# Optimization experiments

Hardware: AMD Instinct MI355X
Metric: run time of the kernel (lower is better)

## Reference

```python
import jax, jax.numpy as jnp
import numpy as np

NUM_CLASSES = 21
GAMMA = 2.0
LAMBDA_WGT = 1.0
EPS = 1e-6  # torch.nn.CosineSimilarity eps
B, C_FEAT, HF, WF = 16, 2048, 41, 41
H, W = 321, 321


def setup_inputs() -> dict:
    key = jax.random.key(0)
    k1, k2, k3, k4, k5 = jax.random.split(key, 5)
    return {
        "y_pred": jax.random.normal(k1, (B, NUM_CLASSES, H, W), dtype=jnp.float32),
        "ycrf": jax.random.randint(k2, (B, H, W), 0, NUM_CLASSES, dtype=jnp.int32),
        "yret": jax.random.randint(k3, (B, H, W), 0, NUM_CLASSES, dtype=jnp.int32),
        "feature_map": jax.random.normal(k4, (B, C_FEAT, HF, WF), dtype=jnp.float32),
        "classifier_weight": jax.random.normal(k5, (NUM_CLASSES, C_FEAT), dtype=jnp.float32),
    }


def reference(y_pred, ycrf, yret, feature_map, classifier_weight):
    K = NUM_CLASSES
    # softmax + log(softmax) fused as log_softmax (original does softmax then log)
    logp = jax.nn.log_softmax(y_pred, axis=1)                    # [B,K,H,W]
    # s_class[b,i,h,w] = (ycrf==i)&(yret==i): nonzero only at i==ycrf when ycrf==yret
    match = (ycrf == yret)                                       # [B,H,W]
    logp_c = jnp.take_along_axis(logp, ycrf[:, None], axis=1)[:, 0]  # [B,H,W] logp at class ycrf
    cnt = jnp.sum(match)
    loss_ce = -jnp.sum(jnp.where(match, logp_c, 0.0)) / cnt

    # correlation map: 1 + cosine(feature_map[b,:,h,w], classifier_weight[i]) at 41x41
    dots = jnp.einsum('bchw,kc->bkhw', feature_map, classifier_weight)   # [B,K,41,41]
    fn = jnp.sqrt(jnp.sum(feature_map * feature_map, axis=1, keepdims=True))  # [B,1,41,41]
    wn = jnp.sqrt(jnp.sum(classifier_weight * classifier_weight, axis=1))     # [K]
    denom_cos = jnp.maximum(fn * wn[None, :, None, None], EPS)
    corr = 1.0 + dots / denom_cos                                # [B,K,41,41]
    # bilinear upsample to 321x321, align_corners=False (half-pixel centers)
    corr_up = jax.image.resize(corr, (B, K, H, W), method='bilinear')
    # confidence map: (corr at class ycrf / max over classes)^gamma
    cstar = jnp.take_along_axis(corr_up, ycrf[:, None], axis=1)[:, 0]   # [B,H,W]
    conf = (cstar / jnp.max(corr_up, axis=1)) ** GAMMA                  # [B,H,W]

    # weighted CE over not_s_class: for each pixel, all classes except the matched one
    # sum_i not_s * conf * logp_i = conf*sum_i logp_i - match*conf*logp_{ycrf}
    m = match.astype(conf.dtype)
    sum_logp = jnp.sum(logp, axis=1)                             # [B,H,W]
    numer = jnp.sum(conf * sum_logp) - jnp.sum(m * conf * logp_c)
    denom = K * jnp.sum(conf) - jnp.sum(m * conf)
    loss_wce = -numer / denom
    return loss_ce + LAMBDA_WGT * loss_wce
```

## Files before the change

kernel.cpp:

```cpp
#include <hip/hip_runtime.h>
#include <math.h>

#define KCLS 21
#define BATCH 16
#define HF 41
#define WF 41
#define HH 321
#define WW 321
#define CFEAT 2048
#define HWF (HF*WF)
#define HWI (HH*WW)
#define NPIX (BATCH*HWI)
#define NBLK_C ((NPIX + 255)/256)
#define EPSC 1e-6f

__device__ float g_wn[KCLS];
__device__ float g_corr[(size_t)BATCH*KCLS*HWF];
__device__ float g_part[6][NBLK_C];

__global__ __launch_bounds__(256) void k_wn(const float* __restrict__ cw) {
    int wave = threadIdx.x >> 6, lane = threadIdx.x & 63;
    for (int k = wave; k < KCLS; k += 4) {
        float s = 0.f;
        for (int c = lane; c < CFEAT; c += 64) {
            float v = cw[k*CFEAT + c];
            s = fmaf(v, v, s);
        }
        #pragma unroll
        for (int off = 32; off; off >>= 1) s += __shfl_down(s, off, 64);
        if (lane == 0) g_wn[k] = sqrtf(s);
    }
}

__global__ __launch_bounds__(512) void k_corr(const float* __restrict__ fm,
                                              const float* __restrict__ cw) {
    int b = blockIdx.y;
    int lane = threadIdx.x & 63;
    int chunk = __builtin_amdgcn_readfirstlane(threadIdx.x >> 6);
    int hw = blockIdx.x * 64 + lane;
    bool valid = hw < HWF;
    const float* fbase = fm + (size_t)b * CFEAT * HWF + (valid ? hw : 0);
    int cbase = chunk * (CFEAT / 8);

    float acc[KCLS];
    #pragma unroll
    for (int k = 0; k < KCLS; ++k) acc[k] = 0.f;
    float nrm = 0.f;

    for (int j = 0; j < CFEAT/8; j += 4) {
        int c = cbase + j;
        float f0 = fbase[(size_t)(c+0)*HWF];
        float f1 = fbase[(size_t)(c+1)*HWF];
        float f2 = fbase[(size_t)(c+2)*HWF];
        float f3 = fbase[(size_t)(c+3)*HWF];
        nrm = fmaf(f0,f0, fmaf(f1,f1, fmaf(f2,f2, fmaf(f3,f3, nrm))));
        #pragma unroll
        for (int k = 0; k < KCLS; ++k) {
            const float4 wv = *reinterpret_cast<const float4*>(cw + (size_t)k*CFEAT + c);
            acc[k] = fmaf(f0,wv.x, fmaf(f1,wv.y, fmaf(f2,wv.z, fmaf(f3,wv.w, acc[k]))));
        }
    }

    __shared__ float red[KCLS+1][8][64];
    #pragma unroll
    for (int k = 0; k < KCLS; ++k) red[k][chunk][lane] = acc[k];
    red[KCLS][chunk][lane] = nrm;
    __syncthreads();

    if (threadIdx.x < 64) {
        int p = lane;
        int hw2 = blockIdx.x * 64 + p;
        if (hw2 < HWF) {
            float n8 = 0.f;
            #pragma unroll
            for (int j = 0; j < 8; ++j) n8 += red[KCLS][j][p];
            float fn = sqrtf(n8);
            float* out = g_corr + (size_t)b * KCLS * HWF + hw2;
            #pragma unroll
            for (int k = 0; k < KCLS; ++k) {
                float d = 0.f;
                #pragma unroll
                for (int j = 0; j < 8; ++j) d += red[k][j][p];
                float den = fmaxf(fn * g_wn[k], EPSC);
                out[(size_t)k * HWF] = 1.f + d / den;
            }
        }
    }
}

__global__ __launch_bounds__(256) void k_main(const float* __restrict__ yp,
                                              const int* __restrict__ ycrf,
                                              const int* __restrict__ yret) {
    int tid = threadIdx.x;
    int p = blockIdx.x * 256 + tid;
    float a0=0.f, a1=0.f, a2=0.f, a3=0.f, a4=0.f, a5=0.f;
    if (p < NPIX) {
        int b = p / HWI;
        int r = p - b * HWI;
        int h = r / WW;
        int w = r - h * WW;
        int c = ycrf[p];
        bool match = (c == yret[p]);

        const float* ybase = yp + (size_t)b * KCLS * HWI + r;
        float v[KCLS];
        float mx = -1e30f, sum_y = 0.f;
        #pragma unroll
        for (int k = 0; k < KCLS; ++k) {
            v[k] = ybase[(size_t)k * HWI];
            sum_y += v[k];
            mx = fmaxf(mx, v[k]);
        }
        float se = 0.f, yc = 0.f;
        #pragma unroll
        for (int k = 0; k < KCLS; ++k) {
            se += __expf(v[k] - mx);
            yc = (k == c) ? v[k] : yc;
        }
        float lse = __logf(se);
        float logp_c = yc - mx - lse;
        float sum_logp = sum_y - (float)KCLS * (mx + lse);

        const float S = (float)HF / (float)HH;
        float xf = ((float)w + 0.5f) * S - 0.5f;
        float yf = ((float)h + 0.5f) * S - 0.5f;
        float xg = floorf(xf), yg = floorf(yf);
        float fx = xf - xg, fy = yf - yg;
        int ix0 = (int)xg; if (ix0 < 0) ix0 = 0;
        int iy0 = (int)yg; if (iy0 < 0) iy0 = 0;
        int ix1 = (int)xg + 1; if (ix1 > WF-1) ix1 = WF-1; if (ix1 < 0) ix1 = 0;
        int iy1 = (int)yg + 1; if (iy1 > HF-1) iy1 = HF-1; if (iy1 < 0) iy1 = 0;
        float w00 = (1.f-fx)*(1.f-fy), w01 = fx*(1.f-fy);
        float w10 = (1.f-fx)*fy,       w11 = fx*fy;
        int o00 = iy0*WF+ix0, o01 = iy0*WF+ix1, o10 = iy1*WF+ix0, o11 = iy1*WF+ix1;

        const float* cb = g_corr + (size_t)b * KCLS * HWF;
        float cmax = -1e30f, cstar = 0.f;
        #pragma unroll
        for (int k = 0; k < KCLS; ++k) {
            const float* ck = cb + (size_t)k * HWF;
            float cv = w00*ck[o00] + w01*ck[o01] + w10*ck[o10] + w11*ck[o11];
            cmax = fmaxf(cmax, cv);
            cstar = (k == c) ? cv : cstar;
        }
        float ratio = cstar / cmax;
        float conf = ratio * ratio;
        float mf = match ? 1.f : 0.f;

        a0 = match ? logp_c : 0.f;
        a1 = mf;
        a2 = conf * sum_logp;
        a3 = mf * conf * logp_c;
        a4 = conf;
        a5 = mf * conf;
    }

    #pragma unroll
    for (int off = 32; off; off >>= 1) {
        a0 += __shfl_down(a0, off, 64);
        a1 += __shfl_down(a1, off, 64);
        a2 += __shfl_down(a2, off, 64);
        a3 += __shfl_down(a3, off, 64);
        a4 += __shfl_down(a4, off, 64);
        a5 += __shfl_down(a5, off, 64);
    }
    __shared__ float s[4][6];
    int wave = tid >> 6, lane = tid & 63;
    if (lane == 0) {
        s[wave][0]=a0; s[wave][1]=a1; s[wave][2]=a2;
        s[wave][3]=a3; s[wave][4]=a4; s[wave][5]=a5;
    }
    __syncthreads();
    if (tid == 0) {
        #pragma unroll
        for (int j = 0; j < 6; ++j)
            g_part[j][blockIdx.x] = s[0][j] + s[1][j] + s[2][j] + s[3][j];
    }
}

__global__ __launch_bounds__(256) void k_final(float* __restrict__ out) {
    int tid = threadIdx.x;
    float s[6] = {0,0,0,0,0,0};
    for (int i = tid; i < NBLK_C; i += 256) {
        #pragma unroll
        for (int j = 0; j < 6; ++j) s[j] += g_part[j][i];
    }
    #pragma unroll
    for (int j = 0; j < 6; ++j) {
        #pragma unroll
        for (int off = 32; off; off >>= 1) s[j] += __shfl_down(s[j], off, 64);
    }
    __shared__ float red[4][6];
    int wave = tid >> 6, lane = tid & 63;
    if (lane == 0) {
        #pragma unroll
        for (int j = 0; j < 6; ++j) red[wave][j] = s[j];
    }
    __syncthreads();
    if (tid == 0) {
        float A    = red[0][0]+red[1][0]+red[2][0]+red[3][0];
        float CNT  = red[0][1]+red[1][1]+red[2][1]+red[3][1];
        float Scs  = red[0][2]+red[1][2]+red[2][2]+red[3][2];
        float Smcl = red[0][3]+red[1][3]+red[2][3]+red[3][3];
        float Sc   = red[0][4]+red[1][4]+red[2][4]+red[3][4];
        float Smc  = red[0][5]+red[1][5]+red[2][5]+red[3][5];
        float loss_ce  = -A / CNT;
        float numer = Scs - Smcl;
        float denom = (float)KCLS * Sc - Smc;
        float loss_wce = -numer / denom;
        out[0] = loss_ce + loss_wce;
    }
}

extern "C" void kernel_launch(void* const* d_in, const int* in_sizes, int n_in,
                              void* d_out, int out_size, void* d_ws, size_t ws_size,
                              hipStream_t stream) {
    const float* y_pred = (const float*)d_in[0];
    const int*   ycrf   = (const int*)d_in[1];
    const int*   yret   = (const int*)d_in[2];
    const float* fm     = (const float*)d_in[3];
    const float* cw     = (const float*)d_in[4];
    float* out = (float*)d_out;

    k_wn  <<<1, 256, 0, stream>>>(cw);
    k_corr<<<dim3((HWF+63)/64, BATCH), 512, 0, stream>>>(fm, cw);
    k_main<<<NBLK_C, 256, 0, stream>>>(y_pred, ycrf, yret);
    k_final<<<1, 256, 0, stream>>>(out);
}
```

Before: 516.7 us.

## Fold weight-norm and final reduction kernels into corr and main kernels

```diff
diff --git a/kernel.cpp b/kernel.cpp
--- a/kernel.cpp
+++ b/kernel.cpp
@@ -14,26 +14,17 @@
 #define NBLK_C ((NPIX + 255)/256)
 #define EPSC 1e-6f
 
-__device__ float g_wn[KCLS];
 __device__ float g_corr[(size_t)BATCH*KCLS*HWF];
-__device__ float g_part[6][NBLK_C];
-
-__global__ __launch_bounds__(256) void k_wn(const float* __restrict__ cw) {
-    int wave = threadIdx.x >> 6, lane = threadIdx.x & 63;
-    for (int k = wave; k < KCLS; k += 4) {
-        float s = 0.f;
-        for (int c = lane; c < CFEAT; c += 64) {
-            float v = cw[k*CFEAT + c];
-            s = fmaf(v, v, s);
-        }
-        #pragma unroll
-        for (int off = 32; off; off >>= 1) s += __shfl_down(s, off, 64);
-        if (lane == 0) g_wn[k] = sqrtf(s);
-    }
-}
+__device__ float g_acc[6];
+__device__ unsigned g_ticket;
 
 __global__ __launch_bounds__(512) void k_corr(const float* __restrict__ fm,
                                               const float* __restrict__ cw) {
+    if (blockIdx.x == 0 && blockIdx.y == 0) {
+        if (threadIdx.x < 6) g_acc[threadIdx.x] = 0.f;
+        if (threadIdx.x == 6) g_ticket = 0u;
+    }
+
     int b = blockIdx.y;
     int lane = threadIdx.x & 63;
     int chunk = __builtin_amdgcn_readfirstlane(threadIdx.x >> 6);
@@ -47,24 +38,41 @@
     for (int k = 0; k < KCLS; ++k) acc[k] = 0.f;
     float nrm = 0.f;
 
-    for (int j = 0; j < CFEAT/8; j += 4) {
+    for (int j = 0; j < CFEAT/8; j += 8) {
         int c = cbase + j;
-        float f0 = fbase[(size_t)(c+0)*HWF];
-        float f1 = fbase[(size_t)(c+1)*HWF];
-        float f2 = fbase[(size_t)(c+2)*HWF];
-        float f3 = fbase[(size_t)(c+3)*HWF];
-        nrm = fmaf(f0,f0, fmaf(f1,f1, fmaf(f2,f2, fmaf(f3,f3, nrm))));
-        #pragma unroll
-        for (int k = 0; k < KCLS; ++k) {
-            const float4 wv = *reinterpret_cast<const float4*>(cw + (size_t)k*CFEAT + c);
-            acc[k] = fmaf(f0,wv.x, fmaf(f1,wv.y, fmaf(f2,wv.z, fmaf(f3,wv.w, acc[k]))));
+        float f[8];
+        #pragma unroll
+        for (int u = 0; u < 8; ++u) f[u] = fbase[(size_t)(c+u)*HWF];
+        #pragma unroll
+        for (int u = 0; u < 8; ++u) nrm = fmaf(f[u], f[u], nrm);
+        #pragma unroll
+        for (int k = 0; k < KCLS; ++k) {
+            const float4 w0 = *reinterpret_cast<const float4*>(cw + (size_t)k*CFEAT + c);
+            const float4 w1 = *reinterpret_cast<const float4*>(cw + (size_t)k*CFEAT + c + 4);
+            acc[k] = fmaf(f[0],w0.x, fmaf(f[1],w0.y, fmaf(f[2],w0.z, fmaf(f[3],w0.w, acc[k]))));
+            acc[k] = fmaf(f[4],w1.x, fmaf(f[5],w1.y, fmaf(f[6],w1.z, fmaf(f[7],w1.w, acc[k]))));
         }
     }
 
     __shared__ float red[KCLS+1][8][64];
+    __shared__ float s_wn[KCLS];
     #pragma unroll
     for (int k = 0; k < KCLS; ++k) red[k][chunk][lane] = acc[k];
     red[KCLS][chunk][lane] = nrm;
+    __syncthreads();
+
+    for (int k = chunk; k < KCLS; k += 8) {
+        float s = 0.f;
+        const float4* row = reinterpret_cast<const float4*>(cw + (size_t)k*CFEAT);
+        #pragma unroll
+        for (int i = 0; i < CFEAT/4/64; ++i) {
+            float4 v4 = row[lane + 64*i];
+            s = fmaf(v4.x,v4.x, fmaf(v4.y,v4.y, fmaf(v4.z,v4.z, fmaf(v4.w,v4.w, s))));
+        }
+        #pragma unroll
+        for (int off = 32; off; off >>= 1) s += __shfl_down(s, off, 64);
+        if (lane == 0) s_wn[k] = sqrtf(s);
+    }
     __syncthreads();
 
     if (threadIdx.x < 64) {
@@ -81,7 +89,7 @@
                 float d = 0.f;
                 #pragma unroll
                 for (int j = 0; j < 8; ++j) d += red[k][j][p];
-                float den = fmaxf(fn * g_wn[k], EPSC);
+                float den = fmaxf(fn * s_wn[k], EPSC);
                 out[(size_t)k * HWF] = 1.f + d / den;
             }
         }
@@ -90,7 +98,8 @@
 
 __global__ __launch_bounds__(256) void k_main(const float* __restrict__ yp,
                                               const int* __restrict__ ycrf,
-                                              const int* __restrict__ yret) {
+                                              const int* __restrict__ yret,
+                                              float* __restrict__ out) {
     int tid = threadIdx.x;
     int p = blockIdx.x * 256 + tid;
     float a0=0.f, a1=0.f, a2=0.f, a3=0.f, a4=0.f, a5=0.f;
@@ -172,43 +181,33 @@
     }
     __syncthreads();
     if (tid == 0) {
-        #pragma unroll
-        for (int j = 0; j < 6; ++j)
-            g_part[j][blockIdx.x] = s[0][j] + s[1][j] + s[2][j] + s[3][j];
-    }
-}
-
-__global__ __launch_bounds__(256) void k_final(float* __restrict__ out) {
-    int tid = threadIdx.x;
-    float s[6] = {0,0,0,0,0,0};
-    for (int i = tid; i < NBLK_C; i += 256) {
-        #pragma unroll
-        for (int j = 0; j < 6; ++j) s[j] += g_part[j][i];
-    }
-    #pragma unroll
-    for (int j = 0; j < 6; ++j) {
-        #pragma unroll
-        for (int off = 32; off; off >>= 1) s[j] += __shfl_down(s[j], off, 64);
-    }
-    __shared__ float red[4][6];
-    int wave = tid >> 6, lane = tid & 63;
-    if (lane == 0) {
-        #pragma unroll
-        for (int j = 0; j < 6; ++j) red[wave][j] = s[j];
-    }
-    __syncthreads();
-    if (tid == 0) {
-        float A    = red[0][0]+red[1][0]+red[2][0]+red[3][0];
-        float CNT  = red[0][1]+red[1][1]+red[2][1]+red[3][1];
-        float Scs  = red[0][2]+red[1][2]+red[2][2]+red[3][2];
-        float Smcl = red[0][3]+red[1][3]+red[2][3]+red[3][3];
-        float Sc   = red[0][4]+red[1][4]+red[2][4]+red[3][4];
-        float Smc  = red[0][5]+red[1][5]+red[2][5]+red[3][5];
-        float loss_ce  = -A / CNT;
-        float numer = Scs - Smcl;
-        float denom = (float)KCLS * Sc - Smc;
-        float loss_wce = -numer / denom;
-        out[0] = loss_ce + loss_wce;
+        float t0 = s[0][0]+s[1][0]+s[2][0]+s[3][0];
+        float t1 = s[0][1]+s[1][1]+s[2][1]+s[3][1];
+        float t2 = s[0][2]+s[1][2]+s[2][2]+s[3][2];
+        float t3 = s[0][3]+s[1][3]+s[2][3]+s[3][3];
+        float t4 = s[0][4]+s[1][4]+s[2][4]+s[3][4];
+        float t5 = s[0][5]+s[1][5]+s[2][5]+s[3][5];
+        atomicAdd(&g_acc[0], t0);
+        atomicAdd(&g_acc[1], t1);
+        atomicAdd(&g_acc[2], t2);
+        atomicAdd(&g_acc[3], t3);
+        atomicAdd(&g_acc[4], t4);
+        atomicAdd(&g_acc[5], t5);
+        __threadfence();
+        unsigned old = atomicAdd(&g_ticket, 1u);
+        if (old == gridDim.x - 1) {
+            float A    = atomicAdd(&g_acc[0], 0.f);
+            float CNT  = atomicAdd(&g_acc[1], 0.f);
+            float Scs  = atomicAdd(&g_acc[2], 0.f);
+            float Smcl = atomicAdd(&g_acc[3], 0.f);
+            float Sc   = atomicAdd(&g_acc[4], 0.f);
+            float Smc  = atomicAdd(&g_acc[5], 0.f);
+            float loss_ce  = -A / CNT;
+            float numer = Scs - Smcl;
+            float denom = (float)KCLS * Sc - Smc;
+            float loss_wce = -numer / denom;
+            out[0] = loss_ce + loss_wce;
+        }
     }
 }
 
@@ -222,8 +221,6 @@
     const float* cw     = (const float*)d_in[4];
     float* out = (float*)d_out;
 
-    k_wn  <<<1, 256, 0, stream>>>(cw);
     k_corr<<<dim3((HWF+63)/64, BATCH), 512, 0, stream>>>(fm, cw);
-    k_main<<<NBLK_C, 256, 0, stream>>>(y_pred, ycrf, yret);
-    k_final<<<1, 256, 0, stream>>>(out);
+    k_main<<<NBLK_C, 256, 0, stream>>>(y_pred, ycrf, yret, out);
 }
```

Result: slower. 762.8 us (+47.6%).
